# Kernel optimization log

Hardware: AMD Instinct MI355X
Metric: run time of the kernel (lower is better)

Reference implementation:

```python
import jax, jax.numpy as jnp
import numpy as np

N_FFT = 1024
N_STAGES = 4
BATCH = 16384


def _mod_seq(order):
    mset = [0]
    for o in range(order):
        step = 2 ** o
        mset = [v for x in mset for v in (x, x + step)]
    return mset


def _partial_bit_reversal(N, order):
    m = np.zeros((N, N), dtype=np.float32)
    base = 2 ** order
    k = 0
    for p in _mod_seq(order):
        for j in range(N // base):
            m[j * base + p, k] = 1.0
            k += 1
    return m


def setup_inputs() -> dict:
    key = jax.random.key(0)
    x = jax.random.normal(key, (BATCH, N_FFT), dtype=jnp.float32)
    n_sub = N_FFT // 2 ** N_STAGES  # 64: dense sub-DFT size
    dft = np.fft.fft(np.eye(n_sub))
    inp = {
        "x": x,
        "perm": jnp.asarray(_partial_bit_reversal(N_FFT, N_STAGES)),
        "fft_real": jnp.asarray(dft.real, dtype=jnp.float32),
        "fft_imag": jnp.asarray(dft.imag, dtype=jnp.float32),
    }
    stage = N_FFT // 2 ** (N_STAGES - 1)  # 128, doubles each stage
    for s in range(N_STAGES):
        w = np.exp(-2j * np.pi / stage) ** np.arange(stage // 2)
        inp[f"tw_real_{s}"] = jnp.asarray(w.real, dtype=jnp.float32)
        inp[f"tw_imag_{s}"] = jnp.asarray(w.imag, dtype=jnp.float32)
        stage *= 2
    return inp


def _fft_forward(x, perm, fft_real, fft_imag, tws):
    # bit-reversal permutation (matmul against 0/1 matrix, as in the original)
    y = x @ perm
    n_chunks = 2 ** N_STAGES
    # stack chunks: (n_chunks, B, n_sub)
    c = jnp.stack(jnp.split(y, n_chunks, axis=-1), axis=0)
    ev, od = c[0::2], c[1::2]  # (m, B, s) each, m = n_chunks // 2
    # dense sub-DFTs (x @ M.T)
    ev_r = jnp.einsum('mbs,ts->mbt', ev, fft_real)
    ev_i = jnp.einsum('mbs,ts->mbt', ev, fft_imag)
    od_r = jnp.einsum('mbs,ts->mbt', od, fft_real)
    od_i = jnp.einsum('mbs,ts->mbt', od, fft_imag)
    # butterfly twiddle stages; m halves and s doubles each stage
    for tr, ti in tws:
        todd_r = tr * od_r - ti * od_i
        todd_i = tr * od_i + ti * od_r
        real = jnp.concatenate([ev_r + todd_r, ev_r - todd_r], axis=-1)
        imag = jnp.concatenate([ev_i + todd_i, ev_i - todd_i], axis=-1)
        ev_r, od_r = real[0::2], real[1::2]
        ev_i, od_i = imag[0::2], imag[1::2]
    return ev_r[0], ev_i[0]


def reference(x, perm, fft_real, fft_imag,
              tw_real_0, tw_imag_0, tw_real_1, tw_imag_1,
              tw_real_2, tw_imag_2, tw_real_3, tw_imag_3):
    tws = [(tw_real_0, tw_imag_0), (tw_real_1, tw_imag_1),
           (tw_real_2, tw_imag_2), (tw_real_3, tw_imag_3)]
    return _fft_forward(x, perm, fft_real, fft_imag, tws)
```

## Files before the change

kernel.cpp:

```cpp
#include <hip/hip_runtime.h>


#define N_FFT 1024
#define BATCH 16384
#define TPB   256

typedef float f4 __attribute__((ext_vector_type(4)));

__device__ __forceinline__ int pad16(int a) { return a + (a >> 4); }

__device__ __forceinline__ float2 cmul(float2 a, float2 b) {
    return make_float2(a.x * b.x - a.y * b.y, a.x * b.y + a.y * b.x);
}

template<int M, int STEP, bool UNIT_TW>
__device__ __forceinline__ void butterfly_store(float2 a, float2 b, float2 c, float2 d,
                                                float2* __restrict__ dst,
                                                const float2* __restrict__ tw,
                                                int tid)
{
    const int j = tid / M;
    const int k = tid % M;
    float2 t0 = make_float2(a.x + c.x, a.y + c.y);
    float2 t1 = make_float2(a.x - c.x, a.y - c.y);
    float2 t2 = make_float2(b.x + d.x, b.y + d.y);
    float2 t3 = make_float2(b.y - d.y, d.x - b.x);
    float2 y0 = make_float2(t0.x + t2.x, t0.y + t2.y);
    float2 u1 = make_float2(t1.x + t3.x, t1.y + t3.y);
    float2 u2 = make_float2(t0.x - t2.x, t0.y - t2.y);
    float2 u3 = make_float2(t1.x - t3.x, t1.y - t3.y);
    const int base = 4 * M * j + k;
    if (UNIT_TW) {
        dst[pad16(base)]         = y0;
        dst[pad16(base + M)]     = u1;
        dst[pad16(base + 2 * M)] = u2;
        dst[pad16(base + 3 * M)] = u3;
    } else {
        float2 w1 = tw[STEP * j];
        float2 w2 = cmul(w1, w1);
        float2 w3 = cmul(w1, w2);
        dst[pad16(base)]         = y0;
        dst[pad16(base + M)]     = cmul(u1, w1);
        dst[pad16(base + 2 * M)] = cmul(u2, w2);
        dst[pad16(base + 3 * M)] = cmul(u3, w3);
    }
}

template<int M, int STEP, bool UNIT_TW>
__device__ __forceinline__ void stage_mid(const float2* __restrict__ src,
                                          float2* __restrict__ dst,
                                          const float2* __restrict__ tw,
                                          int tid)
{
    float2 a = src[pad16(tid)];
    float2 b = src[pad16(tid + 256)];
    float2 c = src[pad16(tid + 512)];
    float2 d = src[pad16(tid + 768)];
    butterfly_store<M, STEP, UNIT_TW>(a, b, c, d, dst, tw, tid);
}

__global__ __launch_bounds__(TPB) void fft1024_kernel(
    const float* __restrict__ x,
    const float* __restrict__ twr,
    const float* __restrict__ twi,
    float* __restrict__ outr,
    float* __restrict__ outi)
{
    __shared__ __align__(16) float2 bufA[1088];
    __shared__ __align__(16) float2 bufB[1088];
    __shared__ __align__(16) float2 tw[256];

    const int tid = threadIdx.x;
    const long long r0 = 2LL * blockIdx.x;

    {
        const f4* __restrict__ xv = reinterpret_cast<const f4*>(x + r0 * N_FFT);
        f4* xs = reinterpret_cast<f4*>(bufB);
        xs[tid]       = xv[tid];
        xs[tid + 256] = xv[tid + 256];
    }
    if (tid < 64) {
        f4 re = reinterpret_cast<const f4*>(twr)[tid];
        f4 im = reinterpret_cast<const f4*>(twi)[tid];
        #pragma unroll
        for (int j = 0; j < 4; ++j)
            tw[4 * tid + j] = make_float2(re[j], im[j]);
    }
    __syncthreads();

    {
        const float* xs = reinterpret_cast<const float*>(bufB);
        float2 a = make_float2(xs[tid],       xs[tid + 1024]);
        float2 b = make_float2(xs[tid + 256], xs[tid + 1280]);
        float2 c = make_float2(xs[tid + 512], xs[tid + 1536]);
        float2 d = make_float2(xs[tid + 768], xs[tid + 1792]);
        butterfly_store<1, 1, false>(a, b, c, d, bufA, tw, tid);
    }
    __syncthreads();

    stage_mid<4, 4, false>(bufA, bufB, tw, tid);
    __syncthreads();
    stage_mid<16, 16, false>(bufB, bufA, tw, tid);
    __syncthreads();
    stage_mid<64, 64, false>(bufA, bufB, tw, tid);
    __syncthreads();
    stage_mid<256, 0, true>(bufB, bufA, tw, tid);
    __syncthreads();

    f4* or0v = reinterpret_cast<f4*>(outr + r0 * N_FFT);
    f4* oi0v = reinterpret_cast<f4*>(outi + r0 * N_FFT);
    f4 vr0, vi0, vr1, vi1;
    #pragma unroll
    for (int j = 0; j < 4; ++j) {
        const int k  = 4 * tid + j;
        const int nk = (N_FFT - k) & (N_FFT - 1);
        float2 zk = bufA[pad16(k)];
        float2 zn = bufA[pad16(nk)];
        vr0[j] = 0.5f * (zk.x + zn.x);
        vi0[j] = 0.5f * (zk.y - zn.y);
        vr1[j] = 0.5f * (zk.y + zn.y);
        vi1[j] = 0.5f * (zn.x - zk.x);
    }
    __builtin_nontemporal_store(vr0, or0v + tid);
    __builtin_nontemporal_store(vi0, oi0v + tid);
    __builtin_nontemporal_store(vr1, or0v + 256 + tid);
    __builtin_nontemporal_store(vi1, oi0v + 256 + tid);
}

extern "C" void kernel_launch(void* const* d_in, const int* in_sizes, int n_in,
                              void* d_out, int out_size, void* d_ws, size_t ws_size,
                              hipStream_t stream) {
    const float* x   = (const float*)d_in[0];
    const float* twr = (const float*)d_in[10];
    const float* twi = (const float*)d_in[11];
    float* outr = (float*)d_out;
    float* outi = outr + (size_t)BATCH * N_FFT;
    fft1024_kernel<<<BATCH / 2, TPB, 0, stream>>>(x, twr, twi, outr, outi);
}
```

Before: 204.7 us.

## Give each wavefront its own FFT pair held in registers, dropping block barriers

Each 64-thread wavefront now computes one two-row real-FFT pair. The data lives in 16 registers per thread, and only three LDS exchanges are needed, guarded by lgkmcnt waits instead of block-wide __syncthreads. Two radix-4 stages run in registers between exchanges. The block handles 8 rows instead of 2, and launch bounds ask for 4 blocks per SU. This removes most block barriers and LDS round-trips, at the cost of more registers and larger per-block LDS (4×1088 float2). The global input loads are now strided scalar loads instead of f4 vectors, and the output stores are less coalesced.

```diff
diff --git a/kernel.cpp b/kernel.cpp
--- a/kernel.cpp
+++ b/kernel.cpp
@@ -12,119 +12,139 @@
 __device__ __forceinline__ float2 cmul(float2 a, float2 b) {
     return make_float2(a.x * b.x - a.y * b.y, a.x * b.y + a.y * b.x);
 }
+__device__ __forceinline__ float2 cadd(float2 a, float2 b) { return make_float2(a.x + b.x, a.y + b.y); }
+__device__ __forceinline__ float2 csub(float2 a, float2 b) { return make_float2(a.x - b.x, a.y - b.y); }
 
-template<int M, int STEP, bool UNIT_TW>
-__device__ __forceinline__ void butterfly_store(float2 a, float2 b, float2 c, float2 d,
-                                                float2* __restrict__ dst,
-                                                const float2* __restrict__ tw,
-                                                int tid)
+#define LDS_FENCE() asm volatile("s_waitcnt lgkmcnt(0)" ::: "memory")
+
+__device__ __forceinline__ void bf4(float2& A, float2& B, float2& C, float2& D, float2 w1)
 {
-    const int j = tid / M;
-    const int k = tid % M;
-    float2 t0 = make_float2(a.x + c.x, a.y + c.y);
-    float2 t1 = make_float2(a.x - c.x, a.y - c.y);
-    float2 t2 = make_float2(b.x + d.x, b.y + d.y);
-    float2 t3 = make_float2(b.y - d.y, d.x - b.x);
-    float2 y0 = make_float2(t0.x + t2.x, t0.y + t2.y);
-    float2 u1 = make_float2(t1.x + t3.x, t1.y + t3.y);
-    float2 u2 = make_float2(t0.x - t2.x, t0.y - t2.y);
-    float2 u3 = make_float2(t1.x - t3.x, t1.y - t3.y);
-    const int base = 4 * M * j + k;
-    if (UNIT_TW) {
-        dst[pad16(base)]         = y0;
-        dst[pad16(base + M)]     = u1;
-        dst[pad16(base + 2 * M)] = u2;
-        dst[pad16(base + 3 * M)] = u3;
-    } else {
-        float2 w1 = tw[STEP * j];
-        float2 w2 = cmul(w1, w1);
-        float2 w3 = cmul(w1, w2);
-        dst[pad16(base)]         = y0;
-        dst[pad16(base + M)]     = cmul(u1, w1);
-        dst[pad16(base + 2 * M)] = cmul(u2, w2);
-        dst[pad16(base + 3 * M)] = cmul(u3, w3);
-    }
+    float2 t0 = cadd(A, C), t1 = csub(A, C);
+    float2 t2 = cadd(B, D);
+    float2 t3 = make_float2(B.y - D.y, D.x - B.x);
+    float2 w2 = cmul(w1, w1);
+    float2 w3 = cmul(w1, w2);
+    A = cadd(t0, t2);
+    B = cmul(cadd(t1, t3), w1);
+    C = cmul(csub(t0, t2), w2);
+    D = cmul(csub(t1, t3), w3);
+}
+__device__ __forceinline__ void bf4_nw(float2& A, float2& B, float2& C, float2& D)
+{
+    float2 t0 = cadd(A, C), t1 = csub(A, C);
+    float2 t2 = cadd(B, D);
+    float2 t3 = make_float2(B.y - D.y, D.x - B.x);
+    A = cadd(t0, t2);
+    B = cadd(t1, t3);
+    C = csub(t0, t2);
+    D = csub(t1, t3);
 }
 
-template<int M, int STEP, bool UNIT_TW>
-__device__ __forceinline__ void stage_mid(const float2* __restrict__ src,
-                                          float2* __restrict__ dst,
-                                          const float2* __restrict__ tw,
-                                          int tid)
-{
-    float2 a = src[pad16(tid)];
-    float2 b = src[pad16(tid + 256)];
-    float2 c = src[pad16(tid + 512)];
-    float2 d = src[pad16(tid + 768)];
-    butterfly_store<M, STEP, UNIT_TW>(a, b, c, d, dst, tw, tid);
-}
-
-__global__ __launch_bounds__(TPB) void fft1024_kernel(
+__global__ __launch_bounds__(TPB, 4) void fft1024_kernel(
     const float* __restrict__ x,
     const float* __restrict__ twr,
     const float* __restrict__ twi,
     float* __restrict__ outr,
     float* __restrict__ outi)
 {
-    __shared__ __align__(16) float2 bufA[1088];
-    __shared__ __align__(16) float2 bufB[1088];
-    __shared__ __align__(16) float2 tw[256];
+    __shared__ __align__(16) float2 exbuf[4][1088];
+    __shared__ __align__(16) float2 tws[256];
 
     const int tid = threadIdx.x;
-    const long long r0 = 2LL * blockIdx.x;
+    const int T   = tid & 63;
+    const int wv  = tid >> 6;
+    float2* __restrict__ ex = exbuf[wv];
 
-    {
-        const f4* __restrict__ xv = reinterpret_cast<const f4*>(x + r0 * N_FFT);
-        f4* xs = reinterpret_cast<f4*>(bufB);
-        xs[tid]       = xv[tid];
-        xs[tid + 256] = xv[tid + 256];
-    }
     if (tid < 64) {
         f4 re = reinterpret_cast<const f4*>(twr)[tid];
         f4 im = reinterpret_cast<const f4*>(twi)[tid];
         #pragma unroll
         for (int j = 0; j < 4; ++j)
-            tw[4 * tid + j] = make_float2(re[j], im[j]);
+            tws[4 * tid + j] = make_float2(re[j], im[j]);
     }
+
+    const long long r0 = 2LL * (4LL * blockIdx.x + wv);
+    const float* __restrict__ x0 = x + r0 * N_FFT;
+    const float* __restrict__ x1 = x0 + N_FFT;
+
+    float2 z[16];
+    #pragma unroll
+    for (int q = 0; q < 16; ++q)
+        z[q] = make_float2(x0[T + 64 * q], x1[T + 64 * q]);
+
     __syncthreads();
 
+    #pragma unroll
+    for (int u = 0; u < 4; ++u)
+        bf4(z[u], z[u + 4], z[u + 8], z[u + 12], tws[T + 64 * u]);
     {
-        const float* xs = reinterpret_cast<const float*>(bufB);
-        float2 a = make_float2(xs[tid],       xs[tid + 1024]);
-        float2 b = make_float2(xs[tid + 256], xs[tid + 1280]);
-        float2 c = make_float2(xs[tid + 512], xs[tid + 1536]);
-        float2 d = make_float2(xs[tid + 768], xs[tid + 1792]);
-        butterfly_store<1, 1, false>(a, b, c, d, bufA, tw, tid);
+        float2 wA = tws[4 * T];
+        #pragma unroll
+        for (int r = 0; r < 4; ++r) {
+            bf4(z[4 * r], z[4 * r + 1], z[4 * r + 2], z[4 * r + 3], wA);
+            ex[pad16(16 * T + r)]      = z[4 * r];
+            ex[pad16(16 * T + 4 + r)]  = z[4 * r + 1];
+            ex[pad16(16 * T + 8 + r)]  = z[4 * r + 2];
+            ex[pad16(16 * T + 12 + r)] = z[4 * r + 3];
+        }
     }
-    __syncthreads();
+    LDS_FENCE();
+    #pragma unroll
+    for (int q = 0; q < 16; ++q)
+        z[q] = ex[pad16(T + 64 * q)];
+    LDS_FENCE();
 
-    stage_mid<4, 4, false>(bufA, bufB, tw, tid);
-    __syncthreads();
-    stage_mid<16, 16, false>(bufB, bufA, tw, tid);
-    __syncthreads();
-    stage_mid<64, 64, false>(bufA, bufB, tw, tid);
-    __syncthreads();
-    stage_mid<256, 0, true>(bufB, bufA, tw, tid);
-    __syncthreads();
+    #pragma unroll
+    for (int u = 0; u < 4; ++u)
+        bf4(z[u], z[u + 4], z[u + 8], z[u + 12], tws[(T + 64 * u) & ~15]);
+    {
+        float2 wB = tws[(T >> 4) << 6];
+        const int base2 = ((T >> 4) << 8) + (T & 15);
+        #pragma unroll
+        for (int p = 0; p < 4; ++p) {
+            bf4(z[4 * p], z[4 * p + 1], z[4 * p + 2], z[4 * p + 3], wB);
+            ex[pad16(base2 + 16 * p)]       = z[4 * p];
+            ex[pad16(base2 + 16 * p + 64)]  = z[4 * p + 1];
+            ex[pad16(base2 + 16 * p + 128)] = z[4 * p + 2];
+            ex[pad16(base2 + 16 * p + 192)] = z[4 * p + 3];
+        }
+    }
+    LDS_FENCE();
+
+    #pragma unroll
+    for (int q = 0; q < 16; ++q)
+        z[q] = ex[pad16(T + 64 * q)];
+    #pragma unroll
+    for (int u = 0; u < 4; ++u) {
+        bf4_nw(z[u], z[u + 4], z[u + 8], z[u + 12]);
+        ex[pad16(T + 64 * u)]       = z[u];
+        ex[pad16(T + 64 * u + 256)] = z[u + 4];
+        ex[pad16(T + 64 * u + 512)] = z[u + 8];
+        ex[pad16(T + 64 * u + 768)] = z[u + 12];
+    }
+    LDS_FENCE();
 
     f4* or0v = reinterpret_cast<f4*>(outr + r0 * N_FFT);
     f4* oi0v = reinterpret_cast<f4*>(outi + r0 * N_FFT);
-    f4 vr0, vi0, vr1, vi1;
     #pragma unroll
-    for (int j = 0; j < 4; ++j) {
-        const int k  = 4 * tid + j;
-        const int nk = (N_FFT - k) & (N_FFT - 1);
-        float2 zk = bufA[pad16(k)];
-        float2 zn = bufA[pad16(nk)];
-        vr0[j] = 0.5f * (zk.x + zn.x);
-        vi0[j] = 0.5f * (zk.y - zn.y);
-        vr1[j] = 0.5f * (zk.y + zn.y);
-        vi1[j] = 0.5f * (zn.x - zk.x);
+    for (int g = 0; g < 4; ++g) {
+        f4 vr0, vi0, vr1, vi1;
+        #pragma unroll
+        for (int e = 0; e < 4; ++e) {
+            const int k  = 16 * T + 4 * g + e;
+            const int nk = (N_FFT - k) & (N_FFT - 1);
+            float2 zk = ex[pad16(k)];
+            float2 zn = ex[pad16(nk)];
+            vr0[e] = 0.5f * (zk.x + zn.x);
+            vi0[e] = 0.5f * (zk.y - zn.y);
+            vr1[e] = 0.5f * (zk.y + zn.y);
+            vi1[e] = 0.5f * (zn.x - zk.x);
+        }
+        __builtin_nontemporal_store(vr0, or0v + 4 * T + g);
+        __builtin_nontemporal_store(vi0, oi0v + 4 * T + g);
+        __builtin_nontemporal_store(vr1, or0v + 256 + 4 * T + g);
+        __builtin_nontemporal_store(vi1, oi0v + 256 + 4 * T + g);
     }
-    __builtin_nontemporal_store(vr0, or0v + tid);
-    __builtin_nontemporal_store(vi0, oi0v + tid);
-    __builtin_nontemporal_store(vr1, or0v + 256 + tid);
-    __builtin_nontemporal_store(vi1, oi0v + 256 + tid);
 }
 
 extern "C" void kernel_launch(void* const* d_in, const int* in_sizes, int n_in,
@@ -135,5 +155,5 @@
     const float* twi = (const float*)d_in[11];
     float* outr = (float*)d_out;
     float* outi = outr + (size_t)BATCH * N_FFT;
-    fft1024_kernel<<<BATCH / 2, TPB, 0, stream>>>(x, twr, twi, outr, outi);
+    fft1024_kernel<<<BATCH / 8, TPB, 0, stream>>>(x, twr, twi, outr, outi);
 }
```

New measurement: 393.2 us. 92.1% more time.
